# Kernel tuning notes

Measured on AMD Instinct MI355X. Metric: run time of the kernel, lower is better.

The kernel has to match this reference:

```python
import jax, jax.numpy as jnp
import numpy as np

N_NODES = 100_000
N_EDGES = 1_600_000
F_DIM = 32


def setup_inputs() -> dict:
    key = jax.random.key(0)
    k1, k2, k3 = jax.random.split(key, 3)
    x = jax.random.normal(k1, (N_NODES, F_DIM), dtype=jnp.float32)
    edge_index = jax.random.randint(k2, (2, N_EDGES), 0, N_NODES, dtype=jnp.int64)
    edge_weight = jax.random.uniform(k3, (N_EDGES,), dtype=jnp.float32)
    w_mp = jnp.array([0.5], dtype=jnp.float32)  # learned scalar parameter
    return {"x": x, "edge_index": edge_index, "edge_weight": edge_weight, "w_mp": w_mp}


def reference(x, edge_index, edge_weight, w_mp):
    # message: ea = w_mp * x[src] * edge_weight  (shape [E, F])
    # aggregate: sum messages into target nodes (aggr='add', source_to_target)
    src = edge_index[0]
    dst = edge_index[1]
    ea = (w_mp * x[src]) * edge_weight[:, None]          # [E, F]
    out = jax.ops.segment_sum(ea, dst, num_segments=x.shape[0])  # [N, F]
    return out
```

## Files before the change

### kernel.cpp

```cpp
#include <hip/hip_runtime.h>


constexpr int N_NODES = 100000;
constexpr int N_EDGES = 1600000;
constexpr int F_DIM   = 32;

constexpr int NPB_C = 256;
constexpr int NB_C  = (N_NODES + NPB_C - 1) / NPB_C;
constexpr int CAP_C = 4608;

constexpr int CUR_STRIDE = 32;

constexpr int BIN_THREADS = 1024;
constexpr int BIN_BLOCKS  = 512;
constexpr int BIN_CHUNK   = N_EDGES / BIN_BLOCKS;
constexpr int BIN_EPT     = (BIN_CHUNK + BIN_THREADS - 1) / BIN_THREADS;

constexpr int AGG_THREADS = 512;
constexpr int GRPT = (CAP_C + AGG_THREADS - 1) / AGG_THREADS;

constexpr size_t WS_CURSOR  = 0;
constexpr size_t WS_RECORDS = 64 * 1024;
constexpr size_t WS_NEEDED  = WS_RECORDS + (size_t)NB_C * CAP_C * 8;
constexpr size_t WS_ZERO    = (size_t)NB_C * CUR_STRIDE * 4;

__global__ __launch_bounds__(BIN_THREADS, 8) void bin_edges(
    const int* __restrict__ src, const int* __restrict__ dst,
    const float* __restrict__ ew, const float* __restrict__ w_mp,
    int* __restrict__ gcursor, uint2* __restrict__ records)
{
    __shared__ uint2 srt[BIN_CHUNK];
    __shared__ unsigned short srtb[BIN_CHUNK];
    __shared__ int lhist[NB_C];
    __shared__ int loff[NB_C];
    __shared__ int lbase[NB_C];
    __shared__ int lcur[NB_C];
    __shared__ int wsum[8];
    __shared__ int wexc[8];

    const int t    = threadIdx.x;
    const int lane = t & 63;
    const int wv   = t >> 6;

    if (t < NB_C) lhist[t] = 0;
    __syncthreads();

    const float w = w_mp[0];
    const int e0    = blockIdx.x * BIN_CHUNK;
    const int e_end = min(e0 + BIN_CHUNK, N_EDGES);
    const int cnt   = e_end - e0;

    int   bkt[BIN_EPT];
    uint2 rec[BIN_EPT];
    #pragma unroll
    for (int i = 0; i < BIN_EPT; ++i) {
        int j = t + i * BIN_THREADS;
        bkt[i] = -1;
        if (j < cnt) {
            int e = e0 + j;
            int d = dst[e];
            int b = d >> 8;
            bkt[i] = b;
            rec[i].x = __float_as_uint(w * ew[e]);
            rec[i].y = (unsigned)src[e] | ((unsigned)(d & 255) << 24);
            atomicAdd(&lhist[b], 1);
        }
    }
    __syncthreads();

    if (t < 448) {
        int v = (t < NB_C) ? lhist[t] : 0;
        int inc = v;
        #pragma unroll
        for (int d = 1; d < 64; d <<= 1) {
            int o = __shfl_up(inc, d, 64);
            if (lane >= d) inc += o;
        }
        if (lane == 63) wsum[wv] = inc;
        if (t < NB_C) loff[t] = inc - v;
    }
    __syncthreads();
    if (t < 64) {
        int v = (t < 7) ? wsum[t] : 0;
        int inc = v;
        #pragma unroll
        for (int d = 1; d < 8; d <<= 1) {
            int o = __shfl_up(inc, d, 64);
            if (t >= d) inc += o;
        }
        if (t < 7) wexc[t] = inc - v;
    }
    __syncthreads();

    if (t < NB_C) {
        int off = loff[t] + wexc[t >> 6];
        int c   = lhist[t];
        int base = c ? atomicAdd(&gcursor[t * CUR_STRIDE], c) : 0;
        lbase[t] = t * CAP_C + base - off;
        lcur[t]  = off;
    }
    __syncthreads();

    #pragma unroll
    for (int i = 0; i < BIN_EPT; ++i) {
        if (bkt[i] >= 0) {
            int s = atomicAdd(&lcur[bkt[i]], 1);
            srt[s]  = rec[i];
            srtb[s] = (unsigned short)bkt[i];
        }
    }
    __syncthreads();

    for (int j = t; j < cnt; j += BIN_THREADS) {
        int b   = srtb[j];
        int pos = lbase[b] + j;
        if (pos < (b + 1) * CAP_C)
            records[pos] = srt[j];
    }
}

__global__ __launch_bounds__(AGG_THREADS, 4) void sort_gather(
    const int*   __restrict__ gcursor,
    const uint2* __restrict__ records,
    const float* __restrict__ x,
    float*       __restrict__ out)
{
    __shared__ uint2 sorted[CAP_C + 8];
    __shared__ int   hist[NPB_C];
    __shared__ int   offs[NPB_C + 1];
    __shared__ int   cursor[NPB_C];

    const int coarse = blockIdx.x;
    const int t      = threadIdx.x;

    if (t < NPB_C) hist[t] = 0;
    if (t < 8) sorted[CAP_C + t] = make_uint2(0u, 0u);
    __syncthreads();

    const int rbase = coarse * CAP_C;
    const int cnt   = min(gcursor[coarse * CUR_STRIDE], CAP_C);

    uint2 rec[GRPT];
    #pragma unroll
    for (int i = 0; i < GRPT; ++i) {
        int j = t + i * AGG_THREADS;
        rec[i].y = 0xFFFFFFFFu;
        if (j < cnt) {
            rec[i] = records[rbase + j];
            atomicAdd(&hist[rec[i].y >> 24], 1);
        }
    }
    __syncthreads();

    if (t < 64) {
        const int b4 = t * 4;
        int h0 = hist[b4], h1 = hist[b4 + 1], h2 = hist[b4 + 2], h3 = hist[b4 + 3];
        int s   = h0 + h1 + h2 + h3;
        int inc = s;
        #pragma unroll
        for (int d = 1; d < 64; d <<= 1) {
            int o = __shfl_up(inc, d, 64);
            if (t >= d) inc += o;
        }
        int base = inc - s;
        offs[b4]     = base;
        offs[b4 + 1] = base + h0;
        offs[b4 + 2] = base + h0 + h1;
        offs[b4 + 3] = base + h0 + h1 + h2;
        cursor[b4]     = base;
        cursor[b4 + 1] = base + h0;
        cursor[b4 + 2] = base + h0 + h1;
        cursor[b4 + 3] = base + h0 + h1 + h2;
        if (t == 63) offs[NPB_C] = inc;
    }
    __syncthreads();

    #pragma unroll
    for (int i = 0; i < GRPT; ++i) {
        if (rec[i].y != 0xFFFFFFFFu) {
            int slot = atomicAdd(&cursor[rec[i].y >> 24], 1);
            sorted[slot] = rec[i];
        }
    }
    __syncthreads();

    const float4* __restrict__ xv = reinterpret_cast<const float4*>(x);
    const unsigned qoff = (unsigned)(t & 7);
    #pragma unroll
    for (int rnd = 0; rnd < 4; ++rnd) {
        const int node  = rnd * (AGG_THREADS / 8) + (t >> 3);
        const int gnode = coarse * NPB_C + node;
        if (gnode >= N_NODES) continue;

        int j  = offs[node];
        const int je = offs[node + 1];
        float4 acc = make_float4(0.f, 0.f, 0.f, 0.f);

        for (; j < je; j += 8) {
            uint2 r[8];
            #pragma unroll
            for (int k = 0; k < 8; ++k) r[k] = sorted[j + k];
            float    c[8];
            unsigned idx[8];
            #pragma unroll
            for (int k = 0; k < 8; ++k) {
                bool valid = (j + k < je);
                c[k]   = valid ? __uint_as_float(r[k].x) : 0.f;
                idx[k] = valid ? ((r[k].y & 0xFFFFFFu) * 8u + qoff) : qoff;
            }
            float4 v[8];
            #pragma unroll
            for (int k = 0; k < 8; ++k) v[k] = xv[idx[k]];
            #pragma unroll
            for (int k = 0; k < 8; ++k) {
                acc.x += c[k] * v[k].x;
                acc.y += c[k] * v[k].y;
                acc.z += c[k] * v[k].z;
                acc.w += c[k] * v[k].w;
            }
        }
        *reinterpret_cast<float4*>(out + (size_t)gnode * F_DIM + qoff * 4) = acc;
    }
}

__global__ __launch_bounds__(256) void gnn_scatter_atomic(
    const float* __restrict__ x, const int* __restrict__ src,
    const int* __restrict__ dst, const float* __restrict__ ew,
    const float* __restrict__ w_mp, float* __restrict__ out)
{
    const float w = w_mp[0];
    int gid = blockIdx.x * blockDim.x + threadIdx.x;
    int e = gid >> 3;
    int qq = (gid & 7) * 4;
    if (e >= N_EDGES) return;
    int s = src[e];
    int d = dst[e];
    float c = w * ew[e];
    const float4 xv = *reinterpret_cast<const float4*>(x + (size_t)s * F_DIM + qq);
    float* op = out + (size_t)d * F_DIM + qq;
    atomicAdd(op + 0, c * xv.x);
    atomicAdd(op + 1, c * xv.y);
    atomicAdd(op + 2, c * xv.z);
    atomicAdd(op + 3, c * xv.w);
}

extern "C" void kernel_launch(void* const* d_in, const int* in_sizes, int n_in,
                              void* d_out, int out_size, void* d_ws, size_t ws_size,
                              hipStream_t stream) {
    const float* x    = (const float*)d_in[0];
    const int*   ei   = (const int*)d_in[1];
    const float* ew   = (const float*)d_in[2];
    const float* w_mp = (const float*)d_in[3];
    float* out = (float*)d_out;

    const int* src = ei;
    const int* dst = ei + N_EDGES;

    if (ws_size < WS_NEEDED) {
        hipMemsetAsync(d_out, 0, (size_t)out_size * sizeof(float), stream);
        int total = N_EDGES * 8;
        gnn_scatter_atomic<<<(total + 255) / 256, 256, 0, stream>>>(
            x, src, dst, ew, w_mp, out);
        return;
    }

    char* ws = (char*)d_ws;
    int*   gcursor = (int*)(ws + WS_CURSOR);
    uint2* records = (uint2*)(ws + WS_RECORDS);

    hipMemsetAsync(gcursor, 0, WS_ZERO, stream);
    bin_edges<<<BIN_BLOCKS, BIN_THREADS, 0, stream>>>(src, dst, ew, w_mp,
                                                      gcursor, records);
    sort_gather<<<NB_C, AGG_THREADS, 0, stream>>>(gcursor, records, x, out);
}
```

Measured before the change: 123.7 us.

## Replace per-bucket counting sort with LDS atomic scatter accumulation

The second kernel drops the in-block histogram, prefix scan and counting sort of edge records by local destination. Instead each group of 8 threads gathers x rows for its edges and accumulates the scaled messages into a padded shared-memory tile with LDS float atomics, then writes the tile out. This removes several barriers and the sort passes, but adds four LDS atomics per float4 with possible contention on popular destinations. Summation order also becomes nondeterministic.

```diff
diff --git a/kernel.cpp b/kernel.cpp
--- a/kernel.cpp
+++ b/kernel.cpp
@@ -17,7 +17,7 @@
 constexpr int BIN_EPT     = (BIN_CHUNK + BIN_THREADS - 1) / BIN_THREADS;
 
 constexpr int AGG_THREADS = 512;
-constexpr int GRPT = (CAP_C + AGG_THREADS - 1) / AGG_THREADS;
+constexpr int TSTRIDE = F_DIM + 4;
 
 constexpr size_t WS_CURSOR  = 0;
 constexpr size_t WS_RECORDS = 64 * 1024;
@@ -119,107 +119,62 @@
     }
 }
 
-__global__ __launch_bounds__(AGG_THREADS, 4) void sort_gather(
+__global__ __launch_bounds__(AGG_THREADS, 4) void scatter_lds(
     const int*   __restrict__ gcursor,
     const uint2* __restrict__ records,
     const float* __restrict__ x,
     float*       __restrict__ out)
 {
-    __shared__ uint2 sorted[CAP_C + 8];
-    __shared__ int   hist[NPB_C];
-    __shared__ int   offs[NPB_C + 1];
-    __shared__ int   cursor[NPB_C];
+    __shared__ float tile[NPB_C * TSTRIDE];
 
     const int coarse = blockIdx.x;
     const int t      = threadIdx.x;
 
-    if (t < NPB_C) hist[t] = 0;
-    if (t < 8) sorted[CAP_C + t] = make_uint2(0u, 0u);
+    for (int i = t; i < NPB_C * TSTRIDE / 4; i += AGG_THREADS)
+        reinterpret_cast<float4*>(tile)[i] = make_float4(0.f, 0.f, 0.f, 0.f);
     __syncthreads();
 
     const int rbase = coarse * CAP_C;
     const int cnt   = min(gcursor[coarse * CUR_STRIDE], CAP_C);
 
-    uint2 rec[GRPT];
-    #pragma unroll
-    for (int i = 0; i < GRPT; ++i) {
-        int j = t + i * AGG_THREADS;
-        rec[i].y = 0xFFFFFFFFu;
-        if (j < cnt) {
-            rec[i] = records[rbase + j];
-            atomicAdd(&hist[rec[i].y >> 24], 1);
-        }
-    }
-    __syncthreads();
-
-    if (t < 64) {
-        const int b4 = t * 4;
-        int h0 = hist[b4], h1 = hist[b4 + 1], h2 = hist[b4 + 2], h3 = hist[b4 + 3];
-        int s   = h0 + h1 + h2 + h3;
-        int inc = s;
-        #pragma unroll
-        for (int d = 1; d < 64; d <<= 1) {
-            int o = __shfl_up(inc, d, 64);
-            if (t >= d) inc += o;
-        }
-        int base = inc - s;
-        offs[b4]     = base;
-        offs[b4 + 1] = base + h0;
-        offs[b4 + 2] = base + h0 + h1;
-        offs[b4 + 3] = base + h0 + h1 + h2;
-        cursor[b4]     = base;
-        cursor[b4 + 1] = base + h0;
-        cursor[b4 + 2] = base + h0 + h1;
-        cursor[b4 + 3] = base + h0 + h1 + h2;
-        if (t == 63) offs[NPB_C] = inc;
-    }
-    __syncthreads();
-
-    #pragma unroll
-    for (int i = 0; i < GRPT; ++i) {
-        if (rec[i].y != 0xFFFFFFFFu) {
-            int slot = atomicAdd(&cursor[rec[i].y >> 24], 1);
-            sorted[slot] = rec[i];
-        }
-    }
-    __syncthreads();
-
+    const int g     = t >> 3;
+    const int lane8 = t & 7;
     const float4* __restrict__ xv = reinterpret_cast<const float4*>(x);
-    const unsigned qoff = (unsigned)(t & 7);
-    #pragma unroll
-    for (int rnd = 0; rnd < 4; ++rnd) {
-        const int node  = rnd * (AGG_THREADS / 8) + (t >> 3);
-        const int gnode = coarse * NPB_C + node;
-        if (gnode >= N_NODES) continue;
-
-        int j  = offs[node];
-        const int je = offs[node + 1];
-        float4 acc = make_float4(0.f, 0.f, 0.f, 0.f);
-
-        for (; j < je; j += 8) {
-            uint2 r[8];
-            #pragma unroll
-            for (int k = 0; k < 8; ++k) r[k] = sorted[j + k];
-            float    c[8];
-            unsigned idx[8];
-            #pragma unroll
-            for (int k = 0; k < 8; ++k) {
-                bool valid = (j + k < je);
-                c[k]   = valid ? __uint_as_float(r[k].x) : 0.f;
-                idx[k] = valid ? ((r[k].y & 0xFFFFFFu) * 8u + qoff) : qoff;
-            }
-            float4 v[8];
-            #pragma unroll
-            for (int k = 0; k < 8; ++k) v[k] = xv[idx[k]];
-            #pragma unroll
-            for (int k = 0; k < 8; ++k) {
-                acc.x += c[k] * v[k].x;
-                acc.y += c[k] * v[k].y;
-                acc.z += c[k] * v[k].z;
-                acc.w += c[k] * v[k].w;
-            }
-        }
-        *reinterpret_cast<float4*>(out + (size_t)gnode * F_DIM + qoff * 4) = acc;
+
+    for (int j0 = 0; j0 < cnt; j0 += 8 * 64) {
+        uint2 r[8];
+        #pragma unroll
+        for (int b = 0; b < 8; ++b) {
+            int j = j0 + b * 64 + g;
+            r[b] = (j < cnt) ? records[rbase + j] : make_uint2(0u, 0u);
+        }
+        float4 v[8];
+        #pragma unroll
+        for (int b = 0; b < 8; ++b)
+            v[b] = xv[(r[b].y & 0xFFFFFFu) * 8u + lane8];
+        #pragma unroll
+        for (int b = 0; b < 8; ++b) {
+            const float c  = __uint_as_float(r[b].x);
+            const int   dl = (int)(r[b].y >> 24);
+            const int   o  = dl * TSTRIDE + lane8 * 4;
+            atomicAdd(&tile[o + 0], c * v[b].x);
+            atomicAdd(&tile[o + 1], c * v[b].y);
+            atomicAdd(&tile[o + 2], c * v[b].z);
+            atomicAdd(&tile[o + 3], c * v[b].w);
+        }
+    }
+    __syncthreads();
+
+    const int gbase = coarse * NPB_C;
+    for (int i = t; i < NPB_C * 8; i += AGG_THREADS) {
+        const int node  = i >> 3;
+        const int q     = i & 7;
+        const int gnode = gbase + node;
+        if (gnode < N_NODES) {
+            const float4 val = *reinterpret_cast<const float4*>(
+                tile + node * TSTRIDE + q * 4);
+            reinterpret_cast<float4*>(out + (size_t)gnode * F_DIM)[q] = val;
+        }
     }
 }
 
@@ -271,5 +226,5 @@
     hipMemsetAsync(gcursor, 0, WS_ZERO, stream);
     bin_edges<<<BIN_BLOCKS, BIN_THREADS, 0, stream>>>(src, dst, ew, w_mp,
                                                       gcursor, records);
-    sort_gather<<<NB_C, AGG_THREADS, 0, stream>>>(gcursor, records, x, out);
-}
+    scatter_lds<<<NB_C, AGG_THREADS, 0, stream>>>(gcursor, records, x, out);
+}
```

Measured after the change: 471.1 us. 3.81x slower.
